# Kernel optimization log

Measured on AMD Instinct MI355X. Metric: run time of the kernel, lower is better.

Reference implementation:

```python
import jax, jax.numpy as jnp
import numpy as np

EPS = 1e-12  # F.normalize default eps


def setup_inputs() -> dict:
    key = jax.random.key(0)
    ks = jax.random.split(key, 6)
    B, C, D, H, W = 8, 192, 24, 24, 24
    heads = 6
    x = jax.random.normal(ks[0], (B, C, D, H, W), dtype=jnp.float32)
    qkv_w = jax.random.normal(ks[1], (3 * C, C), dtype=jnp.float32) * (1.0 / np.sqrt(C))
    qkv_b = jax.random.normal(ks[2], (3 * C,), dtype=jnp.float32) * 0.02
    temperature = jnp.ones((heads, 1, 1), dtype=jnp.float32)
    proj_w = jax.random.normal(ks[3], (C, C), dtype=jnp.float32) * (1.0 / np.sqrt(C))
    proj_b = jax.random.normal(ks[4], (C,), dtype=jnp.float32) * 0.02
    return {"x": x, "qkv_w": qkv_w, "qkv_b": qkv_b, "temperature": temperature,
            "proj_w": proj_w, "proj_b": proj_b}


def _l2norm_lastdim(t):
    n = jnp.sqrt(jnp.sum(t * t, axis=-1, keepdims=True))
    return t / jnp.maximum(n, EPS)


def reference(x, qkv_w, qkv_b, temperature, proj_w, proj_b):
    B, C, D, H, W = x.shape
    N = D * H * W
    heads = temperature.shape[0]
    hd = C // heads
    xf = x.reshape(B, C, N)
    # 1x1x1 Conv3d == per-voxel linear over channels: (B, 3C, N)
    qkv = jnp.einsum('bcn,oc->bon', xf, qkv_w) + qkv_b[None, :, None]
    # Faithful torch reshape of contiguous (B, 3C, N) buffer -> (B, N, 3, heads, hd),
    # then permute(2,0,3,4,1) -> (3, B, heads, hd, N)
    qkv = qkv.reshape(B, N, 3, heads, hd).transpose(2, 0, 3, 4, 1)
    q, k, v = qkv[0], qkv[1], qkv[2]
    q = _l2norm_lastdim(q)
    k = _l2norm_lastdim(k)
    # channel cross-covariance attention: (B, heads, hd, hd)
    attn = jnp.einsum('bhcn,bhdn->bhcd', q, k) * temperature[None]
    attn = jax.nn.softmax(attn, axis=-1)
    out = jnp.einsum('bhcd,bhdn->bhcn', attn, v)          # (B, heads, hd, N)
    out = out.transpose(0, 2, 1, 3).reshape(B, C, D, H, W)  # transpose(1,2) + reshape
    outf = out.reshape(B, C, N)
    y = jnp.einsum('bcn,oc->bon', outf, proj_w) + proj_b[None, :, None]
    return y.reshape(B, C, D, H, W)
```

## Files before the change

kernel.cpp:

```cpp
#include <hip/hip_runtime.h>

#define B_ 8
#define C_ 192
#define N_ 13824
#define HEADS 6
#define HD 32
#define THREEC 576
#define CHUNKS 24

typedef unsigned short ushort_t;
typedef unsigned int uint_t;
typedef __attribute__((ext_vector_type(8))) _Float16 half8;
typedef __attribute__((ext_vector_type(4))) float f32x4;

__device__ __forceinline__ float h2f(ushort_t u) {
  union { ushort_t u; _Float16 h; } c; c.u = u; return (float)c.h;
}
__device__ __forceinline__ ushort_t f2h(float f) {
  union { _Float16 h; ushort_t u; } c; c.h = (_Float16)f; return c.u;
}

__device__ __forceinline__ void gload_lds16(const ushort_t* g, ushort_t* l) {
  __builtin_amdgcn_global_load_lds(
      (const __attribute__((address_space(1))) void*)g,
      (__attribute__((address_space(3))) void*)l, 16, 0, 0);
}

__device__ __forceinline__ int swz_u(int u, int r) {
  return (u & ~7) | ((u & 7) ^ (r & 7));
}

__global__ __launch_bounds__(256) void wconv(const float* __restrict__ w,
                                             ushort_t* __restrict__ wbf) {
  int idx = (blockIdx.x * 256 + threadIdx.x) * 8;
  float4 v0 = *(const float4*)&w[idx];
  float4 v1 = *(const float4*)&w[idx + 4];
  union { ushort_t us[8]; uint4 v; } pk;
  pk.us[0] = f2h(v0.x); pk.us[1] = f2h(v0.y); pk.us[2] = f2h(v0.z); pk.us[3] = f2h(v0.w);
  pk.us[4] = f2h(v1.x); pk.us[5] = f2h(v1.y); pk.us[6] = f2h(v1.z); pk.us[7] = f2h(v1.w);
  *(uint4*)&wbf[idx] = pk.v;
}

__global__ __launch_bounds__(256) void xt_conv(const float* __restrict__ x,
                                               ushort_t* __restrict__ xT) {
  __shared__ ushort_t tile[64 * 200];
  int t = threadIdx.x;
  int n0 = blockIdx.x * 64, b = blockIdx.y;
  const float* xb = x + (size_t)b * C_ * N_;
  int n4 = t & 15, cp = t >> 4;
#pragma unroll
  for (int it = 0; it < 6; ++it) {
    int c = (cp + it * 16) * 2;
    float4 v0 = *(const float4*)&xb[(size_t)c * N_ + n0 + n4 * 4];
    float4 v1 = *(const float4*)&xb[(size_t)(c + 1) * N_ + n0 + n4 * 4];
    float a0[4] = {v0.x, v0.y, v0.z, v0.w};
    float a1[4] = {v1.x, v1.y, v1.z, v1.w};
#pragma unroll
    for (int i = 0; i < 4; ++i) {
      uint_t wd = (uint_t)f2h(a0[i]) | ((uint_t)f2h(a1[i]) << 16);
      *(uint_t*)&tile[(n4 * 4 + i) * 200 + c] = wd;
    }
  }
  __syncthreads();
  ushort_t* xTb = xT + ((size_t)b * N_ + n0) * C_;
  int r = t >> 2, q = t & 3;
#pragma unroll
  for (int j = 0; j < 6; ++j) {
    int chunk = q * 6 + j;
    uint4 v = *(const uint4*)&tile[r * 200 + chunk * 8];
    *(uint4*)&xTb[r * 192 + chunk * 8] = v;
  }
}

__global__ __launch_bounds__(256) void qkv_gemm_mfma(
    const ushort_t* __restrict__ wbf, const ushort_t* __restrict__ xT,
    const float* __restrict__ bias, ushort_t* __restrict__ qkv) {
  __shared__ ushort_t Bs[128 * 192];
  int t = threadIdx.x;
  int bid = blockIdx.x;
  int l = (bid & 7) * 972 + (bid >> 3);
  int o0 = (l % 9) * 64;
  int rest = l / 9;
  int n0 = (rest % 108) * 128;
  int b = rest / 108;
  int w = t >> 6, lane = t & 63;
  int ln16 = lane & 15, q4 = lane >> 4;
  int mrow = (w >> 1) * 32, ncol = (w & 1) * 64;

  const ushort_t* Bsrc = xT + ((size_t)b * N_ + n0) * C_;

#pragma unroll
  for (int j = 0; j < 12; ++j) {
    int f = (w * 12 + j) * 64 + lane;
    int r = f / 24, u = f - r * 24;
    gload_lds16(Bsrc + r * C_ + swz_u(u, r) * 8, &Bs[(w * 12 + j) * 512]);
  }

  const ushort_t* Abase = wbf + (size_t)(o0 + mrow + ln16) * C_ + q4 * 8;
  half8 afrag[6][2];
#pragma unroll
  for (int kk = 0; kk < 6; ++kk)
#pragma unroll
    for (int mi = 0; mi < 2; ++mi)
      afrag[kk][mi] = *(const half8*)(Abase + mi * 16 * C_ + kk * 32);

  float breg[2][4];
#pragma unroll
  for (int mi = 0; mi < 2; ++mi)
#pragma unroll
    for (int r = 0; r < 4; ++r)
      breg[mi][r] = bias[o0 + mrow + mi * 16 + q4 * 4 + r];

  f32x4 acc[2][4];
#pragma unroll
  for (int mi = 0; mi < 2; ++mi)
#pragma unroll
    for (int ni = 0; ni < 4; ++ni) acc[mi][ni] = (f32x4){0.f, 0.f, 0.f, 0.f};

  int ur[6];
#pragma unroll
  for (int kk = 0; kk < 6; ++kk) ur[kk] = swz_u(kk * 4 + q4, ln16);

  __syncthreads();

  __builtin_amdgcn_s_setprio(1);
#pragma unroll
  for (int kk = 0; kk < 6; ++kk) {
    half8 bb[4];
#pragma unroll
    for (int ni = 0; ni < 4; ++ni)
      bb[ni] = *(const half8*)&Bs[(ncol + ni * 16 + ln16) * 192 + ur[kk] * 8];
#pragma unroll
    for (int mi = 0; mi < 2; ++mi)
#pragma unroll
      for (int ni = 0; ni < 4; ++ni)
        acc[mi][ni] = __builtin_amdgcn_mfma_f32_16x16x32_f16(
            afrag[kk][mi], bb[ni], acc[mi][ni], 0, 0, 0);
  }
  __builtin_amdgcn_s_setprio(0);

#pragma unroll
  for (int mi = 0; mi < 2; ++mi)
#pragma unroll
    for (int ni = 0; ni < 4; ++ni)
#pragma unroll
      for (int r = 0; r < 4; ++r) {
        float v = acc[mi][ni][r] + breg[mi][r];
        int o_l = o0 + mrow + mi * 16 + q4 * 4 + r;
        int n_l = ncol + ni * 16 + ln16;
        qkv[(size_t)(b * THREEC + o_l) * N_ + n0 + n_l] = f2h(v);
      }
}

__global__ __launch_bounds__(256) void attn_partial(
    const ushort_t* __restrict__ qkv, float* __restrict__ Spart) {
  __shared__ float sh[4608];
  int t = threadIdx.x;
  int chunk = blockIdx.x, h = blockIdx.y, b = blockIdx.z;
  int j = t & 31, g8 = t >> 5;
  int tg = t >> 6, tl = t & 63;
  int c0 = (tl & 7) * 4, d0 = (tl >> 3) * 4;
  float acc[4][4];
#pragma unroll
  for (int i = 0; i < 4; ++i)
#pragma unroll
    for (int m = 0; m < 4; ++m) acc[i][m] = 0.f;
  float sqq = 0.f, sqk = 0.f;
  const ushort_t* basep = qkv + (size_t)b * THREEC * N_;
  int n2base = chunk * 576;

  for (int p = 0; p < 9; ++p) {
    __syncthreads();
#pragma unroll
    for (int i = 0; i < 8; ++i) {
      int n2l = g8 * 8 + i;
      int n2 = n2base + p * 64 + n2l;
      int o = n2 / 24, r = n2 - o * 24;
      const ushort_t* rp = basep + (size_t)o * N_ + r * THREEC + h * HD + j;
      float qv = h2f(rp[0]);
      float kv = h2f(rp[C_]);
      sh[n2l * 32 + j] = qv;
      sh[2048 + n2l * 32 + j] = kv;
      sqq = fmaf(qv, qv, sqq);
      sqk = fmaf(kv, kv, sqk);
    }
    __syncthreads();
#pragma unroll
    for (int i = 0; i < 16; ++i) {
      int n2l = tg * 16 + i;
      float4 q4 = *(const float4*)&sh[n2l * 32 + c0];
      float4 k4 = *(const float4*)&sh[2048 + n2l * 32 + d0];
      float q[4] = {q4.x, q4.y, q4.z, q4.w};
      float kk[4] = {k4.x, k4.y, k4.z, k4.w};
#pragma unroll
      for (int ii = 0; ii < 4; ++ii)
#pragma unroll
        for (int mm = 0; mm < 4; ++mm)
          acc[ii][mm] = fmaf(q[ii], kk[mm], acc[ii][mm]);
    }
  }
  __syncthreads();
#pragma unroll
  for (int ii = 0; ii < 4; ++ii)
#pragma unroll
    for (int mm = 0; mm < 4; ++mm)
      sh[tg * 1024 + (c0 + ii) * 32 + (d0 + mm)] = acc[ii][mm];
  sh[4096 + g8 * 32 + j] = sqq;
  sh[4352 + g8 * 32 + j] = sqk;
  __syncthreads();

  float* outp = Spart + (size_t)((b * HEADS + h) * CHUNKS + chunk) * 1088;
  for (int e = t; e < 1024; e += 256)
    outp[e] = sh[e] + sh[1024 + e] + sh[2048 + e] + sh[3072 + e];
  if (t < 32) {
    float s = 0.f;
#pragma unroll
    for (int g = 0; g < 8; ++g) s += sh[4096 + g * 32 + t];
    outp[1024 + t] = s;
  } else if (t < 64) {
    int jj = t - 32;
    float s = 0.f;
#pragma unroll
    for (int g = 0; g < 8; ++g) s += sh[4352 + g * 32 + jj];
    outp[1056 + jj] = s;
  }
}

__global__ __launch_bounds__(256) void attn_final(
    const float* __restrict__ Spart, const float* __restrict__ temp,
    const float* __restrict__ proj_w, ushort_t* __restrict__ W2bf) {
  __shared__ float Sl[1024];
  __shared__ float invq[32], invk[32];
  __shared__ float Pl[192 * 33];
  int t = threadIdx.x;
  int h = blockIdx.x, b = blockIdx.y;
  const float* base = Spart + (size_t)((b * HEADS + h) * CHUNKS) * 1088;

  for (int e = t; e < 1024; e += 256) {
    float s = 0.f;
#pragma unroll
    for (int ch = 0; ch < CHUNKS; ++ch) s += base[ch * 1088 + e];
    Sl[e] = s;
  }
  if (t < 64) {
    int jj = t & 31;
    int off = 1024 + (t >> 5) * 32 + jj;
    float s = 0.f;
#pragma unroll
    for (int ch = 0; ch < CHUNKS; ++ch) s += base[ch * 1088 + off];
    float inv = 1.f / fmaxf(sqrtf(s), 1e-12f);
    if (t < 32) invq[jj] = inv; else invk[jj] = inv;
  }
  for (int e = t; e < 6144; e += 256) {
    int co = e >> 5, c = e & 31;
    Pl[co * 33 + c] = proj_w[(size_t)co * C_ + c * HEADS + h];
  }
  __syncthreads();

  {
    int c = t >> 3, l8 = t & 7;
    float tmpv = temp[h];
    float iq = invq[c];
    float lg[4];
#pragma unroll
    for (int m = 0; m < 4; ++m) {
      int d = l8 * 4 + m;
      lg[m] = Sl[c * 32 + d] * iq * invk[d] * tmpv;
    }
    float mx = fmaxf(fmaxf(lg[0], lg[1]), fmaxf(lg[2], lg[3]));
    for (int off = 1; off < 8; off <<= 1) mx = fmaxf(mx, __shfl_xor(mx, off, 8));
    float ex[4]; float ssum = 0.f;
#pragma unroll
    for (int m = 0; m < 4; ++m) { ex[m] = __expf(lg[m] - mx); ssum += ex[m]; }
    for (int off = 1; off < 8; off <<= 1) ssum += __shfl_xor(ssum, off, 8);
    float inv = 1.f / ssum;
#pragma unroll
    for (int m = 0; m < 4; ++m) Sl[c * 32 + l8 * 4 + m] = ex[m] * inv;
  }
  __syncthreads();

  for (int e2 = t; e2 < 6144; e2 += 256) {
    int co = e2 >> 5, d = e2 & 31;
    float s = 0.f;
#pragma unroll
    for (int c = 0; c < 32; ++c)
      s = fmaf(Pl[co * 33 + c], Sl[c * 32 + d], s);
    W2bf[((size_t)b * C_ + co) * C_ + h * HD + d] = f2h(s);
  }
}

__global__ __launch_bounds__(256) void proj_mfma(
    const ushort_t* __restrict__ qkv, const ushort_t* __restrict__ W2bf,
    const float* __restrict__ pb, float* __restrict__ y) {
  __shared__ ushort_t Bs[128 * 192];
  int t = threadIdx.x;
  int bid = blockIdx.x;
  int l = (bid & 7) * 324 + (bid >> 3);
  int o0 = (l % 3) * 64;
  int rest = l / 3;
  int n2_0 = (rest % 108) * 128;
  int b = rest / 108;
  int w = t >> 6, lane = t & 63;
  int ln16 = lane & 15, q4 = lane >> 4;
  int mrow = (w >> 1) * 32, ncol = (w & 1) * 64;

  const ushort_t* basep = qkv + (size_t)b * THREEC * N_;

#pragma unroll
  for (int j = 0; j < 12; ++j) {
    int f = (w * 12 + j) * 64 + lane;
    int r = f / 24, u = f - r * 24;
    int n2 = n2_0 + r;
    int o = n2 / 24, r2 = n2 - o * 24;
    gload_lds16(basep + (size_t)o * N_ + r2 * THREEC + 384 + swz_u(u, r) * 8,
                &Bs[(w * 12 + j) * 512]);
  }

  const ushort_t* Abase = W2bf + ((size_t)b * C_ + o0 + mrow + ln16) * C_ + q4 * 8;
  half8 afrag[6][2];
#pragma unroll
  for (int kk = 0; kk < 6; ++kk)
#pragma unroll
    for (int mi = 0; mi < 2; ++mi)
      afrag[kk][mi] = *(const half8*)(Abase + mi * 16 * C_ + kk * 32);

  float breg[2][4];
#pragma unroll
  for (int mi = 0; mi < 2; ++mi)
#pragma unroll
    for (int r = 0; r < 4; ++r)
      breg[mi][r] = pb[o0 + mrow + mi * 16 + q4 * 4 + r];

  f32x4 acc[2][4];
#pragma unroll
  for (int mi = 0; mi < 2; ++mi)
#pragma unroll
    for (int ni = 0; ni < 4; ++ni) acc[mi][ni] = (f32x4){0.f, 0.f, 0.f, 0.f};

  int ur[6];
#pragma unroll
  for (int kk = 0; kk < 6; ++kk) ur[kk] = swz_u(kk * 4 + q4, ln16);

  __syncthreads();

  __builtin_amdgcn_s_setprio(1);
#pragma unroll
  for (int kk = 0; kk < 6; ++kk) {
    half8 bb[4];
#pragma unroll
    for (int ni = 0; ni < 4; ++ni)
      bb[ni] = *(const half8*)&Bs[(ncol + ni * 16 + ln16) * 192 + ur[kk] * 8];
#pragma unroll
    for (int mi = 0; mi < 2; ++mi)
#pragma unroll
      for (int ni = 0; ni < 4; ++ni)
        acc[mi][ni] = __builtin_amdgcn_mfma_f32_16x16x32_f16(
            afrag[kk][mi], bb[ni], acc[mi][ni], 0, 0, 0);
  }
  __builtin_amdgcn_s_setprio(0);

#pragma unroll
  for (int mi = 0; mi < 2; ++mi)
#pragma unroll
    for (int ni = 0; ni < 4; ++ni)
#pragma unroll
      for (int r = 0; r < 4; ++r) {
        int co_l = o0 + mrow + mi * 16 + q4 * 4 + r;
        int n_l = ncol + ni * 16 + ln16;
        y[((size_t)b * C_ + co_l) * N_ + n2_0 + n_l] =
            acc[mi][ni][r] + breg[mi][r];
      }
}

extern "C" void kernel_launch(void* const* d_in, const int* in_sizes, int n_in,
                              void* d_out, int out_size, void* d_ws, size_t ws_size,
                              hipStream_t stream) {
  const float* x      = (const float*)d_in[0];
  const float* qkv_w  = (const float*)d_in[1];
  const float* qkv_b  = (const float*)d_in[2];
  const float* temp   = (const float*)d_in[3];
  const float* proj_w = (const float*)d_in[4];
  const float* proj_b = (const float*)d_in[5];
  float* y = (float*)d_out;

  char* wp = (char*)d_ws;
  ushort_t* qkv  = (ushort_t*)wp;  wp += (size_t)B_ * THREEC * N_ * 2;
  ushort_t* xT   = (ushort_t*)wp;  wp += (size_t)B_ * N_ * C_ * 2;
  ushort_t* W2bf = (ushort_t*)wp;  wp += (size_t)B_ * C_ * C_ * 2;
  ushort_t* wbf  = (ushort_t*)wp;
  float* Spart   = (float*)xT;

  wconv<<<54, 256, 0, stream>>>(qkv_w, wbf);
  xt_conv<<<dim3(216, B_), 256, 0, stream>>>(x, xT);
  qkv_gemm_mfma<<<7776, 256, 0, stream>>>(wbf, xT, qkv_b, qkv);
  attn_partial<<<dim3(CHUNKS, HEADS, B_), 256, 0, stream>>>(qkv, Spart);
  attn_final<<<dim3(HEADS, B_), 256, 0, stream>>>(Spart, temp, proj_w, W2bf);
  proj_mfma<<<2592, 256, 0, stream>>>(qkv, W2bf, proj_b, y);
}
```

Measured before the change: 307.3 us.

## Fuse x transpose/convert into QKV GEMM and prefetch vectorized loads in attn_partial

Removes the separate xt_conv kernel and xT buffer: each QKV GEMM block now loads fp32 x directly, converts to fp16 and transposes it into padded LDS rows. The aim is to save a kernel launch and the intermediate write/read of xT, at the cost of re-reading and re-converting x for each of the nine output-channel tiles. attn_partial switches to 16-byte vectorized q/k loads with register prefetch of the next chunk and padded LDS rows, to overlap global latency with compute.

```diff
diff --git a/kernel.cpp b/kernel.cpp
--- a/kernel.cpp
+++ b/kernel.cpp
@@ -29,6 +29,8 @@
 __device__ __forceinline__ int swz_u(int u, int r) {
   return (u & ~7) | ((u & 7) ^ (r & 7));
 }
+
+#define LROW 200
 
 __global__ __launch_bounds__(256) void wconv(const float* __restrict__ w,
                                              ushort_t* __restrict__ wbf) {
@@ -41,41 +43,10 @@
   *(uint4*)&wbf[idx] = pk.v;
 }
 
-__global__ __launch_bounds__(256) void xt_conv(const float* __restrict__ x,
-                                               ushort_t* __restrict__ xT) {
-  __shared__ ushort_t tile[64 * 200];
-  int t = threadIdx.x;
-  int n0 = blockIdx.x * 64, b = blockIdx.y;
-  const float* xb = x + (size_t)b * C_ * N_;
-  int n4 = t & 15, cp = t >> 4;
-#pragma unroll
-  for (int it = 0; it < 6; ++it) {
-    int c = (cp + it * 16) * 2;
-    float4 v0 = *(const float4*)&xb[(size_t)c * N_ + n0 + n4 * 4];
-    float4 v1 = *(const float4*)&xb[(size_t)(c + 1) * N_ + n0 + n4 * 4];
-    float a0[4] = {v0.x, v0.y, v0.z, v0.w};
-    float a1[4] = {v1.x, v1.y, v1.z, v1.w};
-#pragma unroll
-    for (int i = 0; i < 4; ++i) {
-      uint_t wd = (uint_t)f2h(a0[i]) | ((uint_t)f2h(a1[i]) << 16);
-      *(uint_t*)&tile[(n4 * 4 + i) * 200 + c] = wd;
-    }
-  }
-  __syncthreads();
-  ushort_t* xTb = xT + ((size_t)b * N_ + n0) * C_;
-  int r = t >> 2, q = t & 3;
-#pragma unroll
-  for (int j = 0; j < 6; ++j) {
-    int chunk = q * 6 + j;
-    uint4 v = *(const uint4*)&tile[r * 200 + chunk * 8];
-    *(uint4*)&xTb[r * 192 + chunk * 8] = v;
-  }
-}
-
 __global__ __launch_bounds__(256) void qkv_gemm_mfma(
-    const ushort_t* __restrict__ wbf, const ushort_t* __restrict__ xT,
+    const float* __restrict__ x, const ushort_t* __restrict__ wbf,
     const float* __restrict__ bias, ushort_t* __restrict__ qkv) {
-  __shared__ ushort_t Bs[128 * 192];
+  __shared__ ushort_t Bs[128 * LROW];
   int t = threadIdx.x;
   int bid = blockIdx.x;
   int l = (bid & 7) * 972 + (bid >> 3);
@@ -87,13 +58,20 @@
   int ln16 = lane & 15, q4 = lane >> 4;
   int mrow = (w >> 1) * 32, ncol = (w & 1) * 64;
 
-  const ushort_t* Bsrc = xT + ((size_t)b * N_ + n0) * C_;
-
-#pragma unroll
-  for (int j = 0; j < 12; ++j) {
-    int f = (w * 12 + j) * 64 + lane;
-    int r = f / 24, u = f - r * 24;
-    gload_lds16(Bsrc + r * C_ + swz_u(u, r) * 8, &Bs[(w * 12 + j) * 512]);
+  const float* xb = x + (size_t)b * C_ * N_ + n0;
+  int n4 = t & 31, cp = t >> 5;
+#pragma unroll
+  for (int it = 0; it < 12; ++it) {
+    int c = (cp + it * 8) * 2;
+    float4 v0 = *(const float4*)&xb[(size_t)c * N_ + n4 * 4];
+    float4 v1 = *(const float4*)&xb[(size_t)(c + 1) * N_ + n4 * 4];
+    float a0[4] = {v0.x, v0.y, v0.z, v0.w};
+    float a1[4] = {v1.x, v1.y, v1.z, v1.w};
+#pragma unroll
+    for (int i = 0; i < 4; ++i) {
+      uint_t wd = (uint_t)f2h(a0[i]) | ((uint_t)f2h(a1[i]) << 16);
+      *(uint_t*)&Bs[(n4 * 4 + i) * LROW + c] = wd;
+    }
   }
 
   const ushort_t* Abase = wbf + (size_t)(o0 + mrow + ln16) * C_ + q4 * 8;
@@ -117,19 +95,16 @@
 #pragma unroll
     for (int ni = 0; ni < 4; ++ni) acc[mi][ni] = (f32x4){0.f, 0.f, 0.f, 0.f};
 
-  int ur[6];
-#pragma unroll
-  for (int kk = 0; kk < 6; ++kk) ur[kk] = swz_u(kk * 4 + q4, ln16);
-
   __syncthreads();
 
   __builtin_amdgcn_s_setprio(1);
 #pragma unroll
   for (int kk = 0; kk < 6; ++kk) {
+    int k0 = kk * 32 + q4 * 8;
     half8 bb[4];
 #pragma unroll
     for (int ni = 0; ni < 4; ++ni)
-      bb[ni] = *(const half8*)&Bs[(ncol + ni * 16 + ln16) * 192 + ur[kk] * 8];
+      bb[ni] = *(const half8*)&Bs[(ncol + ni * 16 + ln16) * LROW + k0];
 #pragma unroll
     for (int mi = 0; mi < 2; ++mi)
 #pragma unroll
@@ -154,12 +129,13 @@
 
 __global__ __launch_bounds__(256) void attn_partial(
     const ushort_t* __restrict__ qkv, float* __restrict__ Spart) {
-  __shared__ float sh[4608];
+  __shared__ float sh[5120];
   int t = threadIdx.x;
   int chunk = blockIdx.x, h = blockIdx.y, b = blockIdx.z;
   int j = t & 31, g8 = t >> 5;
   int tg = t >> 6, tl = t & 63;
   int c0 = (tl & 7) * 4, d0 = (tl >> 3) * 4;
+  int lrow = t >> 2, loct = t & 3;
   float acc[4][4];
 #pragma unroll
   for (int i = 0; i < 4; ++i)
@@ -169,27 +145,49 @@
   const ushort_t* basep = qkv + (size_t)b * THREEC * N_;
   int n2base = chunk * 576;
 
+  uint4 qv4, kv4;
+  {
+    int n2 = n2base + lrow;
+    int o = n2 / 24, r = n2 - o * 24;
+    const ushort_t* rp = basep + (size_t)o * N_ + r * THREEC + h * HD + loct * 8;
+    qv4 = *(const uint4*)rp;
+    kv4 = *(const uint4*)(rp + C_);
+  }
+
   for (int p = 0; p < 9; ++p) {
     __syncthreads();
+    {
+      union { uint4 v; ushort_t us[8]; } uq, uk;
+      uq.v = qv4; uk.v = kv4;
+      float4 qa = {h2f(uq.us[0]), h2f(uq.us[1]), h2f(uq.us[2]), h2f(uq.us[3])};
+      float4 qb = {h2f(uq.us[4]), h2f(uq.us[5]), h2f(uq.us[6]), h2f(uq.us[7])};
+      float4 ka = {h2f(uk.us[0]), h2f(uk.us[1]), h2f(uk.us[2]), h2f(uk.us[3])};
+      float4 kb = {h2f(uk.us[4]), h2f(uk.us[5]), h2f(uk.us[6]), h2f(uk.us[7])};
+      float* dq = &sh[lrow * 36 + loct * 8];
+      float* dk = &sh[2304 + lrow * 36 + loct * 8];
+      *(float4*)dq = qa; *(float4*)(dq + 4) = qb;
+      *(float4*)dk = ka; *(float4*)(dk + 4) = kb;
+    }
+    __syncthreads();
+    if (p < 8) {
+      int n2 = n2base + (p + 1) * 64 + lrow;
+      int o = n2 / 24, r = n2 - o * 24;
+      const ushort_t* rp = basep + (size_t)o * N_ + r * THREEC + h * HD + loct * 8;
+      qv4 = *(const uint4*)rp;
+      kv4 = *(const uint4*)(rp + C_);
+    }
 #pragma unroll
     for (int i = 0; i < 8; ++i) {
-      int n2l = g8 * 8 + i;
-      int n2 = n2base + p * 64 + n2l;
-      int o = n2 / 24, r = n2 - o * 24;
-      const ushort_t* rp = basep + (size_t)o * N_ + r * THREEC + h * HD + j;
-      float qv = h2f(rp[0]);
-      float kv = h2f(rp[C_]);
-      sh[n2l * 32 + j] = qv;
-      sh[2048 + n2l * 32 + j] = kv;
+      float qv = sh[(g8 * 8 + i) * 36 + j];
+      float kv = sh[2304 + (g8 * 8 + i) * 36 + j];
       sqq = fmaf(qv, qv, sqq);
       sqk = fmaf(kv, kv, sqk);
     }
-    __syncthreads();
 #pragma unroll
     for (int i = 0; i < 16; ++i) {
       int n2l = tg * 16 + i;
-      float4 q4 = *(const float4*)&sh[n2l * 32 + c0];
-      float4 k4 = *(const float4*)&sh[2048 + n2l * 32 + d0];
+      float4 q4 = *(const float4*)&sh[n2l * 36 + c0];
+      float4 k4 = *(const float4*)&sh[2304 + n2l * 36 + d0];
       float q[4] = {q4.x, q4.y, q4.z, q4.w};
       float kk[4] = {k4.x, k4.y, k4.z, k4.w};
 #pragma unroll
@@ -205,8 +203,8 @@
 #pragma unroll
     for (int mm = 0; mm < 4; ++mm)
       sh[tg * 1024 + (c0 + ii) * 32 + (d0 + mm)] = acc[ii][mm];
-  sh[4096 + g8 * 32 + j] = sqq;
-  sh[4352 + g8 * 32 + j] = sqk;
+  sh[4608 + g8 * 32 + j] = sqq;
+  sh[4864 + g8 * 32 + j] = sqk;
   __syncthreads();
 
   float* outp = Spart + (size_t)((b * HEADS + h) * CHUNKS + chunk) * 1088;
@@ -215,13 +213,13 @@
   if (t < 32) {
     float s = 0.f;
 #pragma unroll
-    for (int g = 0; g < 8; ++g) s += sh[4096 + g * 32 + t];
+    for (int g = 0; g < 8; ++g) s += sh[4608 + g * 32 + t];
     outp[1024 + t] = s;
   } else if (t < 64) {
     int jj = t - 32;
     float s = 0.f;
 #pragma unroll
-    for (int g = 0; g < 8; ++g) s += sh[4352 + g * 32 + jj];
+    for (int g = 0; g < 8; ++g) s += sh[4864 + g * 32 + jj];
     outp[1056 + jj] = s;
   }
 }
@@ -385,14 +383,12 @@
 
   char* wp = (char*)d_ws;
   ushort_t* qkv  = (ushort_t*)wp;  wp += (size_t)B_ * THREEC * N_ * 2;
-  ushort_t* xT   = (ushort_t*)wp;  wp += (size_t)B_ * N_ * C_ * 2;
+  float* Spart   = (float*)wp;     wp += (size_t)B_ * HEADS * CHUNKS * 1088 * 4;
   ushort_t* W2bf = (ushort_t*)wp;  wp += (size_t)B_ * C_ * C_ * 2;
   ushort_t* wbf  = (ushort_t*)wp;
-  float* Spart   = (float*)xT;
 
   wconv<<<54, 256, 0, stream>>>(qkv_w, wbf);
-  xt_conv<<<dim3(216, B_), 256, 0, stream>>>(x, xT);
-  qkv_gemm_mfma<<<7776, 256, 0, stream>>>(wbf, xT, qkv_b, qkv);
+  qkv_gemm_mfma<<<7776, 256, 0, stream>>>(x, wbf, qkv_b, qkv);
   attn_partial<<<dim3(CHUNKS, HEADS, B_), 256, 0, stream>>>(qkv, Spart);
   attn_final<<<dim3(HEADS, B_), 256, 0, stream>>>(Spart, temp, proj_w, W2bf);
   proj_mfma<<<2592, 256, 0, stream>>>(qkv, W2bf, proj_b, y);
```

Result: slower. 359.1 us (+16.9%).
